# Performance work log

Measured on AMD Instinct MI355X. Metric: run time of the kernel, lower is better.

The kernel has to match this reference:

```python
import jax, jax.numpy as jnp
import numpy as np

PATCH = 3       # patch_size
PAD = PATCH // 2
ITERS = 5       # iterations
RADIUS = 4      # random_search radius


def get_patches(feats, nnf):
    # feats: [b,c,H,W]; nnf: [b,2,h,w] float coords (row, col)
    # Returns per-pixel patches [b,h,w,P,P,c] gathered at rounded, clipped coords
    b, c, H, W = feats.shape
    fp = jnp.pad(feats, ((0, 0), (0, 0), (PAD, PAD), (PAD, PAD)))
    fp = jnp.transpose(fp, (0, 2, 3, 1))  # [b,H+2p,W+2p,c]
    y = jnp.clip(jnp.round(nnf[:, 0]), 0, H - 1).astype(jnp.int32)  # [b,h,w]
    x = jnp.clip(jnp.round(nnf[:, 1]), 0, W - 1).astype(jnp.int32)
    off = jnp.arange(PATCH)
    yy = y[..., None, None] + off[:, None]   # [b,h,w,P,1] (already offset by PAD in padded frame)
    xx = x[..., None, None] + off[None, :]   # [b,h,w,1,P]
    bi = jnp.arange(b)[:, None, None, None, None]
    return fp[bi, yy, xx]  # [b,h,w,P,P,c]


def patch_distance(ps, pt):
    # SSD over patch and channel dims -> [b,h,w]
    return jnp.sum((ps - pt) ** 2, axis=(3, 4, 5))


def propagate(nnf, source, target, direction):
    shifted = jnp.roll(nnf, direction, axis=3)
    cur_d = patch_distance(get_patches(source, nnf), get_patches(target, nnf))
    shf_d = patch_distance(get_patches(source, shifted), get_patches(target, shifted))
    mask = (shf_d < cur_d)[:, None]  # [b,1,h,w]
    return jnp.where(mask, shifted, nnf)


def random_search(nnf, source, target, key):
    hmax = target.shape[2] - 1  # torch code clamps both coords to H-1
    cur_d = patch_distance(get_patches(source, nnf), get_patches(target, nnf))
    for i in range(RADIUS):
        key, k = jax.random.split(key)
        rand_nnf = jnp.clip(
            nnf + jax.random.normal(k, nnf.shape, nnf.dtype) * (2.0 ** (-i)),
            0.0, float(hmax))
        rand_d = patch_distance(get_patches(source, rand_nnf), get_patches(target, rand_nnf))
        mask = rand_d < cur_d  # [b,h,w]
        nnf = jnp.where(mask[:, None], rand_nnf, nnf)
        cur_d = jnp.where(mask, rand_d, cur_d)
    return nnf


def setup_inputs() -> dict:
    key = jax.random.key(0)
    k1, k2 = jax.random.split(key)
    source = jax.random.normal(k1, (2, 32, 256, 256), dtype=jnp.float32)
    target = jax.random.normal(k2, (2, 32, 256, 256), dtype=jnp.float32)
    return {"source": source, "target": target}


def reference(source, target):
    b, c, h, w = source.shape
    k0 = jax.random.key(1)
    k_init, k_loop = jax.random.split(k0)
    # init_nnf: uniform in [0, H_t-1] x [0, W_t-1]
    nnf = jax.random.uniform(k_init, (b, 2, h, w), dtype=source.dtype)
    scale = jnp.array([target.shape[2] - 1, target.shape[3] - 1], source.dtype)
    nnf = nnf * scale[None, :, None, None]
    for t in range(ITERS):
        nnf = propagate(nnf, source, target, 1)
        nnf = propagate(nnf, source, target, -1)
        nnf = random_search(nnf, source, target, jax.random.fold_in(k_loop, t))
    return nnf
```

## Files before the change

kernel.cpp:

```cpp
#include <hip/hip_runtime.h>
#include <stdint.h>

#define DEVFN __device__ __forceinline__

DEVFN float mulf(float a, float b) {
#pragma clang fp contract(off)
  return a * b;
}
DEVFN float addf(float a, float b) {
#pragma clang fp contract(off)
  return a + b;
}
DEVFN float subf(float a, float b) {
#pragma clang fp contract(off)
  return a - b;
}

DEVFN uint32_t tf_bits32(uint32_t k0, uint32_t k1, uint32_t ctr) {
  uint32_t ks2 = k0 ^ k1 ^ 0x1BD11BDAu;
  uint32_t x0 = k0;
  uint32_t x1 = ctr + k1;
#define TFR(d) { x0 += x1; x1 = (x1 << (d)) | (x1 >> (32 - (d))); x1 ^= x0; }
  TFR(13) TFR(15) TFR(26) TFR(6)
  x0 += k1; x1 += ks2 + 1u;
  TFR(17) TFR(29) TFR(16) TFR(24)
  x0 += ks2; x1 += k0 + 2u;
  TFR(13) TFR(15) TFR(26) TFR(6)
  x0 += k0; x1 += k1 + 3u;
  TFR(17) TFR(29) TFR(16) TFR(24)
  x0 += k1; x1 += ks2 + 4u;
  TFR(13) TFR(15) TFR(26) TFR(6)
  x0 += ks2; x1 += k0 + 5u;
#undef TFR
  return x0 ^ x1;
}

DEVFN float xla_cephes_logf(float in) {
  float xv = fmaxf(in, __uint_as_float(0x00800000u));
  uint32_t bits = __float_as_uint(xv);
  int ei = (int)(bits >> 23) - 126;
  float m = __uint_as_float((bits & 0x007FFFFFu) | 0x3F000000u);
  float e = (float)ei;
  const float SQRTHF = __uint_as_float(0x3F3504F3u);
  bool lt = m < SQRTHF;
  float tmp = lt ? m : 0.0f;
  m = subf(m, 1.0f);
  e = subf(e, lt ? 1.0f : 0.0f);
  m = addf(m, tmp);
  float z = mulf(m, m);
  float y = 7.0376836292E-2f;
  y = addf(mulf(y, m), -1.1514610310E-1f);
  y = addf(mulf(y, m),  1.1676998740E-1f);
  y = addf(mulf(y, m), -1.2420140846E-1f);
  y = addf(mulf(y, m),  1.4249322787E-1f);
  y = addf(mulf(y, m), -1.6668057665E-1f);
  y = addf(mulf(y, m),  2.0000714765E-1f);
  y = addf(mulf(y, m), -2.4999993993E-1f);
  y = addf(mulf(y, m),  3.3333331174E-1f);
  y = mulf(y, m);
  y = mulf(y, z);
  y = addf(y, mulf(e, -2.12194440e-4f));
  y = subf(y, mulf(z, 0.5f));
  m = addf(m, y);
  m = addf(m, mulf(e, 0.693359375f));
  return m;
}

DEVFN float xla_log1pf(float a) {
  float large = xla_cephes_logf(addf(a, 1.0f));
  float small = mulf(addf(mulf(-0.5f, a), 1.0f), a);
  return (fabsf(a) < __uint_as_float(0x38D1B717u)) ? small : large;
}

DEVFN float xla_erfinvf(float u) {
  float nxx = -mulf(u, u);
  float w = -xla_log1pf(nxx);
  float p;
  if (w < 5.0f) {
    float s = subf(w, 2.5f);
    p = 2.81022636e-08f;
    p = addf(mulf(p, s), 3.43273939e-07f);
    p = addf(mulf(p, s), -3.5233877e-06f);
    p = addf(mulf(p, s), -4.39150654e-06f);
    p = addf(mulf(p, s), 0.00021858087f);
    p = addf(mulf(p, s), -0.00125372503f);
    p = addf(mulf(p, s), -0.00417768164f);
    p = addf(mulf(p, s), 0.246640727f);
    p = addf(mulf(p, s), 1.50140941f);
  } else {
    float s = subf(__fsqrt_rn(w), 3.0f);
    p = -0.000200214257f;
    p = addf(mulf(p, s), 0.000100950558f);
    p = addf(mulf(p, s), 0.00134934322f);
    p = addf(mulf(p, s), -0.00367342844f);
    p = addf(mulf(p, s), 0.00573950773f);
    p = addf(mulf(p, s), -0.0076224613f);
    p = addf(mulf(p, s), 0.00943887047f);
    p = addf(mulf(p, s), 1.00167406f);
    p = addf(mulf(p, s), 2.83297682f);
  }
  return mulf(p, u);
}

DEVFN float unitf(uint32_t bits) {
  return subf(__uint_as_float((bits >> 9) | 0x3F800000u), 1.0f);
}

DEVFN float jax_normal(uint32_t bits) {
  float f = unitf(bits);
  const float lo = __uint_as_float(0xBF7FFFFFu);
  float u = fmaxf(lo, addf(mulf(f, 2.0f), lo));
  const float sqrt2 = __uint_as_float(0x3FB504F3u);
  return mulf(sqrt2, xla_erfinvf(u));
}

struct PMKeys {
  uint32_t ki0, ki1;
  uint32_t sk[5][4][2];
};
struct NK { uint32_t k[20][2]; };

DEVFN float candf(float base, float n, float sig) {
  return fminf(fmaxf(addf(base, mulf(n, sig)), 0.0f), 255.0f);
}
DEVFN int addr_of(float yy, float xx) {
  int iy = (int)rintf(yy);
  int ix = (int)rintf(xx);
  iy = min(max(iy, 0), 255);
  ix = min(max(ix, 0), 255);
  return iy * 256 + ix;
}


__global__ __launch_bounds__(256) void qdiff_n(const float4* __restrict__ S4,
                                               const float4* __restrict__ T4,
                                               float4* __restrict__ Q4,
                                               float* __restrict__ N,
                                               NK nk) {
  __shared__ float lds[64 * 33];
  const int t = threadIdx.x;
  const int bid = blockIdx.x;
  const int xcd = bid & 7;
  const int slot = bid >> 3;
  const int r = xcd * 64 + (slot >> 2);
  const int q = slot & 3;
  const int b = r >> 8;
  const int y = r & 255;
  const int x0 = q << 6;
  const int c = t >> 3;
  const int j0 = t & 7;

  const size_t fbase = (size_t)(b * 32 + c) * 16384 + (size_t)y * 64 + (x0 >> 2);
  float4 s0 = S4[fbase + j0];
  float4 s1 = S4[fbase + j0 + 8];
  float4 t0 = T4[fbase + j0];
  float4 t1 = T4[fbase + j0 + 8];

  uint32_t gtid = (uint32_t)bid * 256u + (uint32_t)t;
#pragma unroll
  for (int i = 0; i < 10; ++i) {
    uint32_t L = (uint32_t)i * 524288u + gtid;
    uint32_t ts = L >> 18;
    uint32_t idx = L & 262143u;
    N[L] = jax_normal(tf_bits32(nk.k[ts][0], nk.k[ts][1], idx));
  }

  {
    float d;
    int p0 = (j0 << 2) * 33 + c;
    d = subf(s0.x, t0.x); lds[p0]           = mulf(d, d);
    d = subf(s0.y, t0.y); lds[p0 + 33]      = mulf(d, d);
    d = subf(s0.z, t0.z); lds[p0 + 66]      = mulf(d, d);
    d = subf(s0.w, t0.w); lds[p0 + 99]      = mulf(d, d);
    int p1 = ((j0 + 8) << 2) * 33 + c;
    d = subf(s1.x, t1.x); lds[p1]           = mulf(d, d);
    d = subf(s1.y, t1.y); lds[p1 + 33]      = mulf(d, d);
    d = subf(s1.z, t1.z); lds[p1 + 66]      = mulf(d, d);
    d = subf(s1.w, t1.w); lds[p1 + 99]      = mulf(d, d);
  }
  __syncthreads();
  const size_t base4 = (((size_t)b * 256 + y) * 8) * 256;
#pragma unroll
  for (int k = 0; k < 2; ++k) {
    int cq = (k << 2) + (t >> 6);
    int px = t & 63;
    int lb = px * 33 + cq * 4;
    float4 v;
    v.x = lds[lb];
    v.y = lds[lb + 1];
    v.z = lds[lb + 2];
    v.w = lds[lb + 3];
    Q4[base4 + (size_t)cq * 256 + x0 + px] = v;
  }
}

__global__ __launch_bounds__(256) void dsum3(const float4* __restrict__ Q4,
                                             float* __restrict__ D) {
  const int x = threadIdx.x;
  const int bid = blockIdx.x;
  const int swz = (bid & 7) * 64 + (bid >> 3);
  const int y = swz & 255;
  const int b = swz >> 8;
  const float4* Qb = Q4 + (size_t)b * 524288;

  float acc = 0.0f;
#pragma unroll 1
  for (int py = 0; py < 3; ++py) {
    int yy = y + py - 1;
    if (yy < 0 || yy > 255) continue;
    const float4* Qrow = Qb + (size_t)yy * 2048;
#pragma unroll 1
    for (int px = 0; px < 3; ++px) {
      int xx = x + px - 1;
      if (xx < 0 || xx > 255) continue;
      float4 v0 = Qrow[xx];
      float4 v1 = Qrow[256 + xx];
      float4 v2 = Qrow[512 + xx];
      float4 v3 = Qrow[768 + xx];
      float4 v4 = Qrow[1024 + xx];
      float4 v5 = Qrow[1280 + xx];
      float4 v6 = Qrow[1536 + xx];
      float4 v7 = Qrow[1792 + xx];
      acc = addf(acc, v0.x); acc = addf(acc, v0.y); acc = addf(acc, v0.z); acc = addf(acc, v0.w);
      acc = addf(acc, v1.x); acc = addf(acc, v1.y); acc = addf(acc, v1.z); acc = addf(acc, v1.w);
      acc = addf(acc, v2.x); acc = addf(acc, v2.y); acc = addf(acc, v2.z); acc = addf(acc, v2.w);
      acc = addf(acc, v3.x); acc = addf(acc, v3.y); acc = addf(acc, v3.z); acc = addf(acc, v3.w);
      acc = addf(acc, v4.x); acc = addf(acc, v4.y); acc = addf(acc, v4.z); acc = addf(acc, v4.w);
      acc = addf(acc, v5.x); acc = addf(acc, v5.y); acc = addf(acc, v5.z); acc = addf(acc, v5.w);
      acc = addf(acc, v6.x); acc = addf(acc, v6.y); acc = addf(acc, v6.z); acc = addf(acc, v6.w);
      acc = addf(acc, v7.x); acc = addf(acc, v7.y); acc = addf(acc, v7.z); acc = addf(acc, v7.w);
    }
  }
  D[(b * 256 + y) * 256 + x] = acc;
}

__global__ __launch_bounds__(256) void pm_fast(const float* __restrict__ D,
                                               const float* __restrict__ N,
                                               float* __restrict__ out,
                                               uint32_t ki0, uint32_t ki1) {
  const int j = threadIdx.x;
  const int bb = blockIdx.x >> 8;
  const int i = blockIdx.x & 255;
  const float* Db = D + bb * 65536;
  __shared__ float sy[256], sx[256];

  const uint32_t idx_y = (uint32_t)(bb * 131072 + i * 256 + j);
  const uint32_t idx_x = idx_y + 65536u;

  float nyv[20], nxv[20];
#pragma unroll
  for (int ts = 0; ts < 20; ++ts) {
    nyv[ts] = N[(size_t)ts * 262144 + idx_y];
    nxv[ts] = N[(size_t)ts * 262144 + idx_x];
  }

  float y = mulf(unitf(tf_bits32(ki0, ki1, idx_y)), 255.0f);
  float x = mulf(unitf(tf_bits32(ki0, ki1, idx_x)), 255.0f);

  float curd = Db[addr_of(y, x)];
#pragma unroll
  for (int t = 0; t < 5; ++t) {
    sy[j] = y; sx[j] = x;
    __syncthreads();
    {
      int jn = (j + 255) & 255;
      float yn = sy[jn], xn = sx[jn];
      float shf = Db[addr_of(yn, xn)];
      if (shf < curd) { y = yn; x = xn; curd = shf; }
    }
    __syncthreads();
    sy[j] = y; sx[j] = x;
    __syncthreads();
    {
      int jn = (j + 1) & 255;
      float yn = sy[jn], xn = sx[jn];
      float shf = Db[addr_of(yn, xn)];
      if (shf < curd) { y = yn; x = xn; curd = shf; }
    }
    __syncthreads();

    float n0y = nyv[t * 4 + 0], n0x = nxv[t * 4 + 0];
    float n1y = nyv[t * 4 + 1], n1x = nxv[t * 4 + 1];
    float n2y = nyv[t * 4 + 2], n2x = nxv[t * 4 + 2];
    float n3y = nyv[t * 4 + 3], n3x = nxv[t * 4 + 3];

    float c0y = candf(y, n0y, 1.0f),  c0x = candf(x, n0x, 1.0f);
    float c1Ay = candf(y,   n1y, 0.5f), c1Ax = candf(x,   n1x, 0.5f);
    float c1By = candf(c0y, n1y, 0.5f), c1Bx = candf(c0x, n1x, 0.5f);
    float c2_0y = candf(y,    n2y, 0.25f), c2_0x = candf(x,    n2x, 0.25f);
    float c2_1y = candf(c1Ay, n2y, 0.25f), c2_1x = candf(c1Ax, n2x, 0.25f);
    float c2_2y = candf(c0y,  n2y, 0.25f), c2_2x = candf(c0x,  n2x, 0.25f);
    float c2_3y = candf(c1By, n2y, 0.25f), c2_3x = candf(c1Bx, n2x, 0.25f);
    float c3_0y = candf(y,     n3y, 0.125f), c3_0x = candf(x,     n3x, 0.125f);
    float c3_1y = candf(c2_0y, n3y, 0.125f), c3_1x = candf(c2_0x, n3x, 0.125f);
    float c3_2y = candf(c1Ay,  n3y, 0.125f), c3_2x = candf(c1Ax,  n3x, 0.125f);
    float c3_3y = candf(c2_1y, n3y, 0.125f), c3_3x = candf(c2_1x, n3x, 0.125f);
    float c3_4y = candf(c0y,   n3y, 0.125f), c3_4x = candf(c0x,   n3x, 0.125f);
    float c3_5y = candf(c2_2y, n3y, 0.125f), c3_5x = candf(c2_2x, n3x, 0.125f);
    float c3_6y = candf(c1By,  n3y, 0.125f), c3_6x = candf(c1Bx,  n3x, 0.125f);
    float c3_7y = candf(c2_3y, n3y, 0.125f), c3_7x = candf(c2_3x, n3x, 0.125f);

    float d0   = Db[addr_of(c0y,  c0x)];
    float d1A  = Db[addr_of(c1Ay, c1Ax)];
    float d1B  = Db[addr_of(c1By, c1Bx)];
    float d2_0 = Db[addr_of(c2_0y, c2_0x)];
    float d2_1 = Db[addr_of(c2_1y, c2_1x)];
    float d2_2 = Db[addr_of(c2_2y, c2_2x)];
    float d2_3 = Db[addr_of(c2_3y, c2_3x)];
    float d3_0 = Db[addr_of(c3_0y, c3_0x)];
    float d3_1 = Db[addr_of(c3_1y, c3_1x)];
    float d3_2 = Db[addr_of(c3_2y, c3_2x)];
    float d3_3 = Db[addr_of(c3_3y, c3_3x)];
    float d3_4 = Db[addr_of(c3_4y, c3_4x)];
    float d3_5 = Db[addr_of(c3_5y, c3_5x)];
    float d3_6 = Db[addr_of(c3_6y, c3_6x)];
    float d3_7 = Db[addr_of(c3_7y, c3_7x)];

    bool a0 = d0 < curd;
    y = a0 ? c0y : y;  x = a0 ? c0x : x;  curd = a0 ? d0 : curd;

    float s1y = a0 ? c1By : c1Ay, s1x = a0 ? c1Bx : c1Ax, s1d = a0 ? d1B : d1A;
    bool a1 = s1d < curd;
    y = a1 ? s1y : y;  x = a1 ? s1x : x;  curd = a1 ? s1d : curd;

    float s2y = a0 ? (a1 ? c2_3y : c2_2y) : (a1 ? c2_1y : c2_0y);
    float s2x = a0 ? (a1 ? c2_3x : c2_2x) : (a1 ? c2_1x : c2_0x);
    float s2d = a0 ? (a1 ? d2_3 : d2_2) : (a1 ? d2_1 : d2_0);
    bool a2 = s2d < curd;
    y = a2 ? s2y : y;  x = a2 ? s2x : x;  curd = a2 ? s2d : curd;

    float s3y = a0 ? (a1 ? (a2 ? c3_7y : c3_6y) : (a2 ? c3_5y : c3_4y))
                   : (a1 ? (a2 ? c3_3y : c3_2y) : (a2 ? c3_1y : c3_0y));
    float s3x = a0 ? (a1 ? (a2 ? c3_7x : c3_6x) : (a2 ? c3_5x : c3_4x))
                   : (a1 ? (a2 ? c3_3x : c3_2x) : (a2 ? c3_1x : c3_0x));
    float s3d = a0 ? (a1 ? (a2 ? d3_7 : d3_6) : (a2 ? d3_5 : d3_4))
                   : (a1 ? (a2 ? d3_3 : d3_2) : (a2 ? d3_1 : d3_0));
    bool a3 = s3d < curd;
    y = a3 ? s3y : y;  x = a3 ? s3x : x;  curd = a3 ? s3d : curd;
  }
  out[idx_y] = y;
  out[idx_x] = x;
}


__global__ __launch_bounds__(256) void compute_d(const float* __restrict__ S,
                                                 const float* __restrict__ T,
                                                 float* __restrict__ D) {
  const int x = threadIdx.x;
  const int y = blockIdx.x & 255;
  const int b = blockIdx.x >> 8;
  const int chs = 65536;
  const float* Sb = S + (size_t)b * 32 * chs;
  const float* Tb = T + (size_t)b * 32 * chs;
  float acc = 0.0f;
  for (int py = 0; py < 3; ++py) {
    int yy = y + py - 1;
    if (yy < 0 || yy > 255) continue;
    for (int px = 0; px < 3; ++px) {
      int xx = x + px - 1;
      if (xx < 0 || xx > 255) continue;
      int off = yy * 256 + xx;
      for (int c = 0; c < 32; ++c) {
        float d = subf(Sb[c * chs + off], Tb[c * chs + off]);
        acc = addf(acc, mulf(d, d));
      }
    }
  }
  D[b * chs + y * 256 + x] = acc;
}

__global__ __launch_bounds__(256) void pm_kernel(const float* __restrict__ D,
                                                 float* __restrict__ out,
                                                 PMKeys K) {
  const int j = threadIdx.x;
  const int bb = blockIdx.x >> 8;
  const int i = blockIdx.x & 255;
  const float* Db = D + bb * 65536;
  __shared__ float sy[256], sx[256];

  const uint32_t idx_y = (uint32_t)(bb * 131072 + i * 256 + j);
  const uint32_t idx_x = idx_y + 65536u;

  float y = mulf(unitf(tf_bits32(K.ki0, K.ki1, idx_y)), 255.0f);
  float x = mulf(unitf(tf_bits32(K.ki0, K.ki1, idx_x)), 255.0f);

  auto lookup = [&](float yy, float xx) -> float {
    int iy = (int)rintf(yy);
    int ix = (int)rintf(xx);
    iy = min(max(iy, 0), 255);
    ix = min(max(ix, 0), 255);
    return Db[iy * 256 + ix];
  };

  for (int t = 0; t < 5; ++t) {
    sy[j] = y; sx[j] = x;
    __syncthreads();
    {
      int jn = (j + 255) & 255;
      float yn = sy[jn], xn = sx[jn];
      float cur = lookup(y, x);
      float shf = lookup(yn, xn);
      if (shf < cur) { y = yn; x = xn; }
    }
    __syncthreads();
    sy[j] = y; sx[j] = x;
    __syncthreads();
    {
      int jn = (j + 1) & 255;
      float yn = sy[jn], xn = sx[jn];
      float cur = lookup(y, x);
      float shf = lookup(yn, xn);
      if (shf < cur) { y = yn; x = xn; }
    }
    __syncthreads();
    float cur = lookup(y, x);
    float sigma = 1.0f;
    for (int s = 0; s < 4; ++s) {
      uint32_t kk0 = K.sk[t][s][0], kk1 = K.sk[t][s][1];
      float ny = jax_normal(tf_bits32(kk0, kk1, idx_y));
      float nx = jax_normal(tf_bits32(kk0, kk1, idx_x));
      float ry = fminf(fmaxf(addf(y, mulf(ny, sigma)), 0.0f), 255.0f);
      float rx = fminf(fmaxf(addf(x, mulf(nx, sigma)), 0.0f), 255.0f);
      float rd = lookup(ry, rx);
      if (rd < cur) { y = ry; x = rx; cur = rd; }
      sigma *= 0.5f;
    }
  }
  out[idx_y] = y;
  out[idx_x] = x;
}

static void h_tf(uint32_t k0, uint32_t k1, uint32_t x0, uint32_t x1,
                 uint32_t& o0, uint32_t& o1) {
  uint32_t ks2 = k0 ^ k1 ^ 0x1BD11BDAu;
  x0 += k0; x1 += k1;
#define HR(d) { x0 += x1; x1 = (x1 << (d)) | (x1 >> (32 - (d))); x1 ^= x0; }
  HR(13) HR(15) HR(26) HR(6)
  x0 += k1; x1 += ks2 + 1u;
  HR(17) HR(29) HR(16) HR(24)
  x0 += ks2; x1 += k0 + 2u;
  HR(13) HR(15) HR(26) HR(6)
  x0 += k0; x1 += k1 + 3u;
  HR(17) HR(29) HR(16) HR(24)
  x0 += k1; x1 += ks2 + 4u;
  HR(13) HR(15) HR(26) HR(6)
  x0 += ks2; x1 += k0 + 5u;
#undef HR
  o0 = x0; o1 = x1;
}

extern "C" void kernel_launch(void* const* d_in, const int* in_sizes, int n_in,
                              void* d_out, int out_size, void* d_ws, size_t ws_size,
                              hipStream_t stream) {
  const float* S = (const float*)d_in[0];
  const float* T = (const float*)d_in[1];
  float* out = (float*)d_out;

  PMKeys K;
  uint32_t kl0, kl1;
  h_tf(0u, 1u, 0u, 0u, K.ki0, K.ki1);
  h_tf(0u, 1u, 0u, 1u, kl0, kl1);
  for (uint32_t t = 0; t < 5; ++t) {
    uint32_t c0, c1;
    h_tf(kl0, kl1, 0u, t, c0, c1);
    for (int s = 0; s < 4; ++s) {
      uint32_t n0, n1, s0, s1;
      h_tf(c0, c1, 0u, 0u, n0, n1);
      h_tf(c0, c1, 0u, 1u, s0, s1);
      K.sk[t][s][0] = s0; K.sk[t][s][1] = s1;
      c0 = n0; c1 = n1;
    }
  }

  const size_t D_BYTES = 2ull * 65536 * 4;
  const size_t Q_BYTES = 2ull * 65536 * 32 * 4;
  const size_t N_BYTES = 20ull * 262144 * 4;
  const size_t NEED = D_BYTES + Q_BYTES + N_BYTES;

  if (ws_size >= NEED) {
    float* Dd = (float*)d_ws;
    float4* Qq = (float4*)((char*)d_ws + D_BYTES);
    float* Nn = (float*)((char*)d_ws + D_BYTES + Q_BYTES);
    NK nk;
    for (int t = 0; t < 5; ++t)
      for (int s = 0; s < 4; ++s) {
        nk.k[t * 4 + s][0] = K.sk[t][s][0];
        nk.k[t * 4 + s][1] = K.sk[t][s][1];
      }
    hipLaunchKernelGGL(qdiff_n, dim3(2048), dim3(256), 0, stream,
                       (const float4*)S, (const float4*)T, Qq, Nn, nk);
    hipLaunchKernelGGL(dsum3, dim3(512), dim3(256), 0, stream, Qq, Dd);
    hipLaunchKernelGGL(pm_fast, dim3(512), dim3(256), 0, stream, Dd, Nn, out, K.ki0, K.ki1);
  } else {
    float* Dd = (float*)d_ws;
    hipLaunchKernelGGL(compute_d, dim3(512), dim3(256), 0, stream, S, T, Dd);
    hipLaunchKernelGGL(pm_kernel, dim3(512), dim3(256), 0, stream, Dd, out, K);
  }
}
```

Measured before the change: 118.2 us.

## Fuse three kernels into one cooperative persistent kernel with grid syncs

Replaces the three-launch pipeline (qdiff/normal generation, 3x3 patch sum, PatchMatch search) with one cooperative kernel of 1024 blocks that uses grid.sync between phases. The aim is to remove launch gaps and inter-kernel drain. In exchange, the patch-sum phase runs on only half the threads of each block and the search phase on half the blocks, which may lower parallelism. The host also adds occupancy and attribute queries on every call.

After: 118.1 us. No clear change (-0.1%).

```diff
diff --git a/kernel.cpp b/kernel.cpp
--- a/kernel.cpp
+++ b/kernel.cpp
@@ -1,4 +1,5 @@
 #include <hip/hip_runtime.h>
+#include <hip/hip_cooperative_groups.h>
 #include <stdint.h>
 
 #define DEVFN __device__ __forceinline__
@@ -131,6 +132,214 @@
   return iy * 256 + ix;
 }
 
+__global__ __launch_bounds__(256, 4) void mega(const float4* __restrict__ S4,
+                                               const float4* __restrict__ T4,
+                                               float4* __restrict__ Q4,
+                                               float* __restrict__ N,
+                                               float* __restrict__ D,
+                                               float* __restrict__ out,
+                                               NK nk, uint32_t ki0, uint32_t ki1) {
+  cooperative_groups::grid_group grid = cooperative_groups::this_grid();
+  __shared__ float lds[64 * 33];
+  const int tid = threadIdx.x;
+  const int bid = blockIdx.x;
+
+  const uint32_t gtid = (uint32_t)bid * 256u + (uint32_t)tid;
+#pragma unroll 1
+  for (int k = 0; k < 2; ++k) {
+    const int g = bid * 2 + k;
+    const int b = g >> 10;
+    const int y = (g >> 2) & 255;
+    const int x0 = (g & 3) << 6;
+    const int c = tid >> 3;
+    const int j0 = tid & 7;
+    const size_t fbase = (size_t)(b * 32 + c) * 16384 + (size_t)y * 64 + (x0 >> 2);
+    float4 s0 = S4[fbase + j0];
+    float4 s1 = S4[fbase + j0 + 8];
+    float4 t0 = T4[fbase + j0];
+    float4 t1 = T4[fbase + j0 + 8];
+
+#pragma unroll
+    for (int i = 0; i < 10; ++i) {
+      int ts = k * 10 + i;
+      N[(size_t)ts * 262144 + gtid] = jax_normal(tf_bits32(nk.k[ts][0], nk.k[ts][1], gtid));
+    }
+
+    {
+      float d;
+      int p0 = (j0 << 2) * 33 + c;
+      d = subf(s0.x, t0.x); lds[p0]      = mulf(d, d);
+      d = subf(s0.y, t0.y); lds[p0 + 33] = mulf(d, d);
+      d = subf(s0.z, t0.z); lds[p0 + 66] = mulf(d, d);
+      d = subf(s0.w, t0.w); lds[p0 + 99] = mulf(d, d);
+      int p1 = ((j0 + 8) << 2) * 33 + c;
+      d = subf(s1.x, t1.x); lds[p1]      = mulf(d, d);
+      d = subf(s1.y, t1.y); lds[p1 + 33] = mulf(d, d);
+      d = subf(s1.z, t1.z); lds[p1 + 66] = mulf(d, d);
+      d = subf(s1.w, t1.w); lds[p1 + 99] = mulf(d, d);
+    }
+    __syncthreads();
+    const size_t base4 = (((size_t)b * 256 + y) * 8) * 256;
+#pragma unroll
+    for (int kk = 0; kk < 2; ++kk) {
+      int cq = (kk << 2) + (tid >> 6);
+      int px = tid & 63;
+      int lb = px * 33 + cq * 4;
+      float4 v;
+      v.x = lds[lb]; v.y = lds[lb + 1]; v.z = lds[lb + 2]; v.w = lds[lb + 3];
+      Q4[base4 + (size_t)cq * 256 + x0 + px] = v;
+    }
+    __syncthreads();
+  }
+
+  grid.sync();
+
+  if (tid < 128) {
+    const int P = bid * 128 + tid;
+    const int b = P >> 16;
+    const int rem = P & 65535;
+    const int y = rem >> 8;
+    const int x = rem & 255;
+    const float4* Qb = Q4 + (size_t)b * 524288;
+    float acc = 0.0f;
+#pragma unroll 1
+    for (int py = 0; py < 3; ++py) {
+      int yy = y + py - 1;
+      if (yy < 0 || yy > 255) continue;
+      const float4* Qrow = Qb + (size_t)yy * 2048;
+#pragma unroll 1
+      for (int px = 0; px < 3; ++px) {
+        int xx = x + px - 1;
+        if (xx < 0 || xx > 255) continue;
+        float4 v0 = Qrow[xx];
+        float4 v1 = Qrow[256 + xx];
+        float4 v2 = Qrow[512 + xx];
+        float4 v3 = Qrow[768 + xx];
+        float4 v4 = Qrow[1024 + xx];
+        float4 v5 = Qrow[1280 + xx];
+        float4 v6 = Qrow[1536 + xx];
+        float4 v7 = Qrow[1792 + xx];
+        acc = addf(acc, v0.x); acc = addf(acc, v0.y); acc = addf(acc, v0.z); acc = addf(acc, v0.w);
+        acc = addf(acc, v1.x); acc = addf(acc, v1.y); acc = addf(acc, v1.z); acc = addf(acc, v1.w);
+        acc = addf(acc, v2.x); acc = addf(acc, v2.y); acc = addf(acc, v2.z); acc = addf(acc, v2.w);
+        acc = addf(acc, v3.x); acc = addf(acc, v3.y); acc = addf(acc, v3.z); acc = addf(acc, v3.w);
+        acc = addf(acc, v4.x); acc = addf(acc, v4.y); acc = addf(acc, v4.z); acc = addf(acc, v4.w);
+        acc = addf(acc, v5.x); acc = addf(acc, v5.y); acc = addf(acc, v5.z); acc = addf(acc, v5.w);
+        acc = addf(acc, v6.x); acc = addf(acc, v6.y); acc = addf(acc, v6.z); acc = addf(acc, v6.w);
+        acc = addf(acc, v7.x); acc = addf(acc, v7.y); acc = addf(acc, v7.z); acc = addf(acc, v7.w);
+      }
+    }
+    D[P] = acc;
+  }
+
+  grid.sync();
+
+  if (bid >= 512) return;
+  float* sy = lds;
+  float* sx = lds + 256;
+  const int j = tid;
+  const int bb = bid >> 8;
+  const int i = bid & 255;
+  const float* Db = D + bb * 65536;
+
+  const uint32_t idx_y = (uint32_t)(bb * 131072 + i * 256 + j);
+  const uint32_t idx_x = idx_y + 65536u;
+
+  float nyv[20], nxv[20];
+#pragma unroll
+  for (int ts = 0; ts < 20; ++ts) {
+    nyv[ts] = N[(size_t)ts * 262144 + idx_y];
+    nxv[ts] = N[(size_t)ts * 262144 + idx_x];
+  }
+
+  float y = mulf(unitf(tf_bits32(ki0, ki1, idx_y)), 255.0f);
+  float x = mulf(unitf(tf_bits32(ki0, ki1, idx_x)), 255.0f);
+
+  float curd = Db[addr_of(y, x)];
+#pragma unroll 1
+  for (int t = 0; t < 5; ++t) {
+    sy[j] = y; sx[j] = x;
+    __syncthreads();
+    {
+      int jn = (j + 255) & 255;
+      float yn = sy[jn], xn = sx[jn];
+      float shf = Db[addr_of(yn, xn)];
+      if (shf < curd) { y = yn; x = xn; curd = shf; }
+    }
+    __syncthreads();
+    sy[j] = y; sx[j] = x;
+    __syncthreads();
+    {
+      int jn = (j + 1) & 255;
+      float yn = sy[jn], xn = sx[jn];
+      float shf = Db[addr_of(yn, xn)];
+      if (shf < curd) { y = yn; x = xn; curd = shf; }
+    }
+    __syncthreads();
+
+    float n0y = nyv[t * 4 + 0], n0x = nxv[t * 4 + 0];
+    float n1y = nyv[t * 4 + 1], n1x = nxv[t * 4 + 1];
+    float n2y = nyv[t * 4 + 2], n2x = nxv[t * 4 + 2];
+    float n3y = nyv[t * 4 + 3], n3x = nxv[t * 4 + 3];
+
+    float c0y = candf(y, n0y, 1.0f),  c0x = candf(x, n0x, 1.0f);
+    float c1Ay = candf(y,   n1y, 0.5f), c1Ax = candf(x,   n1x, 0.5f);
+    float c1By = candf(c0y, n1y, 0.5f), c1Bx = candf(c0x, n1x, 0.5f);
+    float c2_0y = candf(y,    n2y, 0.25f), c2_0x = candf(x,    n2x, 0.25f);
+    float c2_1y = candf(c1Ay, n2y, 0.25f), c2_1x = candf(c1Ax, n2x, 0.25f);
+    float c2_2y = candf(c0y,  n2y, 0.25f), c2_2x = candf(c0x,  n2x, 0.25f);
+    float c2_3y = candf(c1By, n2y, 0.25f), c2_3x = candf(c1Bx, n2x, 0.25f);
+    float c3_0y = candf(y,     n3y, 0.125f), c3_0x = candf(x,     n3x, 0.125f);
+    float c3_1y = candf(c2_0y, n3y, 0.125f), c3_1x = candf(c2_0x, n3x, 0.125f);
+    float c3_2y = candf(c1Ay,  n3y, 0.125f), c3_2x = candf(c1Ax,  n3x, 0.125f);
+    float c3_3y = candf(c2_1y, n3y, 0.125f), c3_3x = candf(c2_1x, n3x, 0.125f);
+    float c3_4y = candf(c0y,   n3y, 0.125f), c3_4x = candf(c0x,   n3x, 0.125f);
+    float c3_5y = candf(c2_2y, n3y, 0.125f), c3_5x = candf(c2_2x, n3x, 0.125f);
+    float c3_6y = candf(c1By,  n3y, 0.125f), c3_6x = candf(c1Bx,  n3x, 0.125f);
+    float c3_7y = candf(c2_3y, n3y, 0.125f), c3_7x = candf(c2_3x, n3x, 0.125f);
+
+    float d0   = Db[addr_of(c0y,  c0x)];
+    float d1A  = Db[addr_of(c1Ay, c1Ax)];
+    float d1B  = Db[addr_of(c1By, c1Bx)];
+    float d2_0 = Db[addr_of(c2_0y, c2_0x)];
+    float d2_1 = Db[addr_of(c2_1y, c2_1x)];
+    float d2_2 = Db[addr_of(c2_2y, c2_2x)];
+    float d2_3 = Db[addr_of(c2_3y, c2_3x)];
+    float d3_0 = Db[addr_of(c3_0y, c3_0x)];
+    float d3_1 = Db[addr_of(c3_1y, c3_1x)];
+    float d3_2 = Db[addr_of(c3_2y, c3_2x)];
+    float d3_3 = Db[addr_of(c3_3y, c3_3x)];
+    float d3_4 = Db[addr_of(c3_4y, c3_4x)];
+    float d3_5 = Db[addr_of(c3_5y, c3_5x)];
+    float d3_6 = Db[addr_of(c3_6y, c3_6x)];
+    float d3_7 = Db[addr_of(c3_7y, c3_7x)];
+
+    bool a0 = d0 < curd;
+    y = a0 ? c0y : y;  x = a0 ? c0x : x;  curd = a0 ? d0 : curd;
+
+    float s1y = a0 ? c1By : c1Ay, s1x = a0 ? c1Bx : c1Ax, s1d = a0 ? d1B : d1A;
+    bool a1 = s1d < curd;
+    y = a1 ? s1y : y;  x = a1 ? s1x : x;  curd = a1 ? s1d : curd;
+
+    float s2y = a0 ? (a1 ? c2_3y : c2_2y) : (a1 ? c2_1y : c2_0y);
+    float s2x = a0 ? (a1 ? c2_3x : c2_2x) : (a1 ? c2_1x : c2_0x);
+    float s2d = a0 ? (a1 ? d2_3 : d2_2) : (a1 ? d2_1 : d2_0);
+    bool a2 = s2d < curd;
+    y = a2 ? s2y : y;  x = a2 ? s2x : x;  curd = a2 ? s2d : curd;
+
+    float s3y = a0 ? (a1 ? (a2 ? c3_7y : c3_6y) : (a2 ? c3_5y : c3_4y))
+                   : (a1 ? (a2 ? c3_3y : c3_2y) : (a2 ? c3_1y : c3_0y));
+    float s3x = a0 ? (a1 ? (a2 ? c3_7x : c3_6x) : (a2 ? c3_5x : c3_4x))
+                   : (a1 ? (a2 ? c3_3x : c3_2x) : (a2 ? c3_1x : c3_0x));
+    float s3d = a0 ? (a1 ? (a2 ? d3_7 : d3_6) : (a2 ? d3_5 : d3_4))
+                   : (a1 ? (a2 ? d3_3 : d3_2) : (a2 ? d3_1 : d3_0));
+    bool a3 = s3d < curd;
+    y = a3 ? s3y : y;  x = a3 ? s3x : x;  curd = a3 ? s3d : curd;
+  }
+  out[idx_y] = y;
+  out[idx_x] = x;
+}
+
 
 __global__ __launch_bounds__(256) void qdiff_n(const float4* __restrict__ S4,
                                                const float4* __restrict__ T4,
@@ -168,15 +377,15 @@
   {
     float d;
     int p0 = (j0 << 2) * 33 + c;
-    d = subf(s0.x, t0.x); lds[p0]           = mulf(d, d);
-    d = subf(s0.y, t0.y); lds[p0 + 33]      = mulf(d, d);
-    d = subf(s0.z, t0.z); lds[p0 + 66]      = mulf(d, d);
-    d = subf(s0.w, t0.w); lds[p0 + 99]      = mulf(d, d);
+    d = subf(s0.x, t0.x); lds[p0]      = mulf(d, d);
+    d = subf(s0.y, t0.y); lds[p0 + 33] = mulf(d, d);
+    d = subf(s0.z, t0.z); lds[p0 + 66] = mulf(d, d);
+    d = subf(s0.w, t0.w); lds[p0 + 99] = mulf(d, d);
     int p1 = ((j0 + 8) << 2) * 33 + c;
-    d = subf(s1.x, t1.x); lds[p1]           = mulf(d, d);
-    d = subf(s1.y, t1.y); lds[p1 + 33]      = mulf(d, d);
-    d = subf(s1.z, t1.z); lds[p1 + 66]      = mulf(d, d);
-    d = subf(s1.w, t1.w); lds[p1 + 99]      = mulf(d, d);
+    d = subf(s1.x, t1.x); lds[p1]      = mulf(d, d);
+    d = subf(s1.y, t1.y); lds[p1 + 33] = mulf(d, d);
+    d = subf(s1.z, t1.z); lds[p1 + 66] = mulf(d, d);
+    d = subf(s1.w, t1.w); lds[p1 + 99] = mulf(d, d);
   }
   __syncthreads();
   const size_t base4 = (((size_t)b * 256 + y) * 8) * 256;
@@ -186,10 +395,7 @@
     int px = t & 63;
     int lb = px * 33 + cq * 4;
     float4 v;
-    v.x = lds[lb];
-    v.y = lds[lb + 1];
-    v.z = lds[lb + 2];
-    v.w = lds[lb + 3];
+    v.x = lds[lb]; v.y = lds[lb + 1]; v.z = lds[lb + 2]; v.w = lds[lb + 3];
     Q4[base4 + (size_t)cq * 256 + x0 + px] = v;
   }
 }
@@ -342,7 +548,6 @@
   out[idx_x] = x;
 }
 
-
 __global__ __launch_bounds__(256) void compute_d(const float* __restrict__ S,
                                                  const float* __restrict__ T,
                                                  float* __restrict__ D) {
@@ -487,10 +692,26 @@
         nk.k[t * 4 + s][0] = K.sk[t][s][0];
         nk.k[t * 4 + s][1] = K.sk[t][s][1];
       }
-    hipLaunchKernelGGL(qdiff_n, dim3(2048), dim3(256), 0, stream,
-                       (const float4*)S, (const float4*)T, Qq, Nn, nk);
-    hipLaunchKernelGGL(dsum3, dim3(512), dim3(256), 0, stream, Qq, Dd);
-    hipLaunchKernelGGL(pm_fast, dim3(512), dim3(256), 0, stream, Dd, Nn, out, K.ki0, K.ki1);
+
+    int coop = 0, dev = 0, maxb = 0;
+    hipGetDevice(&dev);
+    hipDeviceGetAttribute(&coop, hipDeviceAttributeCooperativeLaunch, dev);
+    hipOccupancyMaxActiveBlocksPerMultiprocessor(&maxb, (const void*)mega, 256, 0);
+
+    if (coop && maxb >= 4) {
+      const float4* S4 = (const float4*)S;
+      const float4* T4 = (const float4*)T;
+      uint32_t ki0 = K.ki0, ki1 = K.ki1;
+      void* args[] = {(void*)&S4, (void*)&T4, (void*)&Qq, (void*)&Nn,
+                      (void*)&Dd, (void*)&out, (void*)&nk, (void*)&ki0, (void*)&ki1};
+      hipLaunchCooperativeKernel((const void*)mega, dim3(1024), dim3(256),
+                                 args, 0, stream);
+    } else {
+      hipLaunchKernelGGL(qdiff_n, dim3(2048), dim3(256), 0, stream,
+                         (const float4*)S, (const float4*)T, Qq, Nn, nk);
+      hipLaunchKernelGGL(dsum3, dim3(512), dim3(256), 0, stream, Qq, Dd);
+      hipLaunchKernelGGL(pm_fast, dim3(512), dim3(256), 0, stream, Dd, Nn, out, K.ki0, K.ki1);
+    }
   } else {
     float* Dd = (float*)d_ws;
     hipLaunchKernelGGL(compute_d, dim3(512), dim3(256), 0, stream, S, T, Dd);
```
